# Kernel optimization log

Hardware: AMD Instinct MI355X
Metric: run time of the kernel (lower is better)

## Reference

```python
import jax, jax.numpy as jnp
import numpy as np

CHANNELS = 256

def setup_inputs() -> dict:
    key = jax.random.key(0)
    k1, k2, k3, k4 = jax.random.split(key, 4)
    B, C, N = 16, CHANNELS, 2048
    x = jax.random.normal(k1, (B, C, N), dtype=jnp.float32)
    # Conv1d(C, C, 1) weights are [C_out, C_in] after squeezing kernel dim.
    scale = 1.0 / np.sqrt(C)
    Wqk = jax.random.uniform(k2, (C, C), dtype=jnp.float32, minval=-scale, maxval=scale)  # shared q/k weight
    Wv = jax.random.uniform(k3, (C, C), dtype=jnp.float32, minval=-scale, maxval=scale)
    bv = jax.random.uniform(k4, (C,), dtype=jnp.float32, minval=-scale, maxval=scale)
    return {"x": x, "Wqk": Wqk, "Wv": Wv, "bv": bv}

def reference(x, Wqk, Wv, bv):
    # x: [B, C, N]; q_conv and k_conv share Wqk (tied in the torch module)
    C = x.shape[1]
    dk = jnp.asarray(C, x.dtype) ** 0.5
    x_q = jnp.einsum('oc,bcn->bno', Wqk, x)          # [B, N, C]
    x_k = jnp.einsum('oc,bcn->bon', Wqk, x)          # [B, C, N]
    x_v = jnp.einsum('oc,bcn->bon', Wv, x) + bv[None, :, None]  # [B, C, N]
    energy = jnp.einsum('bnc,bcm->bnm', x_q, x_k)    # [B, N, N]
    attention = jax.nn.softmax(energy, axis=-1)
    # offset-attention renorm: divide by column sums (dim=1), then by sqrt(C)
    attention = attention / (1e-9 + attention.sum(axis=1, keepdims=True))
    attention = attention / dk
    out = jnp.einsum('bcn,bnm->bcm', x_v, attention)  # [B, C, N]
    return out
```

## Files before the change

### kernel.cpp

```cpp
#include <hip/hip_runtime.h>


#define BB 16
#define CC 256
#define NN 2048

typedef float f4 __attribute__((ext_vector_type(4)));
typedef _Float16 h8 __attribute__((ext_vector_type(8)));
typedef _Float16 h4 __attribute__((ext_vector_type(4)));
typedef unsigned int u32;

#define SQRT_LOG2E 1.2011224087864498f
#define WSHIFT 128.0f
#define MFMA16(a, b, c) __builtin_amdgcn_mfma_f32_16x16x32_f16(a, b, c, 0, 0, 0)

__device__ __forceinline__ void glds16(const void* g, void* l) {
    __builtin_amdgcn_global_load_lds(
        (const __attribute__((address_space(1))) u32*)g,
        (__attribute__((address_space(3))) u32*)l, 16, 0, 0);
}

__global__ __launch_bounds__(64)
void convw_kernel(const float* __restrict__ Wqk, const float* __restrict__ Wv,
                  _Float16* __restrict__ Wh, _Float16* __restrict__ Wl)
{
    const int o = blockIdx.x;
    const int t = threadIdx.x;
    const float s = (o < CC) ? SQRT_LOG2E : 1.0f;
    const float* src = (o < CC) ? (Wqk + (size_t)o * CC) : (Wv + (size_t)(o - CC) * CC);
    f4 w = *(const f4*)(src + t * 4);
    h4 hh, hl;
#pragma unroll
    for (int q = 0; q < 4; ++q) {
        float v = s * w[q];
        _Float16 h = (_Float16)v;
        hh[q] = h;
        hl[q] = (_Float16)(v - (float)h);
    }
    *(h4*)(Wh + (size_t)o * CC + t * 4) = hh;
    *(h4*)(Wl + (size_t)o * CC + t * 4) = hl;
}

__global__ __launch_bounds__(256)
void transx_kernel(const float* __restrict__ X, _Float16* __restrict__ Xh,
                   _Float16* __restrict__ Xl)
{
    __shared__ float T[64][65];
    const int t = threadIdx.x;
    const int n0 = blockIdx.x * 64, c0 = blockIdx.y * 64, b = blockIdx.z;
    const float* Xb = X + (size_t)b * CC * NN;
    const int nq = (t & 15) * 4;
    const int cl = t >> 4;
#pragma unroll
    for (int cp = 0; cp < 64; cp += 16) {
        f4 v = *(const f4*)(Xb + (size_t)(c0 + cp + cl) * NN + n0 + nq);
#pragma unroll
        for (int q = 0; q < 4; ++q) T[nq + q][cp + cl] = v[q];
    }
    __syncthreads();
    const int n = t & 63, cq = (t >> 6) * 16;
    _Float16* dh = Xh + ((size_t)b * NN + n0 + n) * CC + c0 + cq;
    _Float16* dl = Xl + ((size_t)b * NN + n0 + n) * CC + c0 + cq;
#pragma unroll
    for (int g = 0; g < 2; ++g) {
        h8 hh, hl;
#pragma unroll
        for (int q = 0; q < 8; ++q) {
            float v = T[n][cq + g * 8 + q];
            _Float16 h = (_Float16)v;
            hh[q] = h;
            hl[q] = (_Float16)(v - (float)h);
        }
        *(h8*)(dh + g * 8) = hh;
        *(h8*)(dl + g * 8) = hl;
    }
}

__global__ __launch_bounds__(512, 4)
void proj_kernel(const _Float16* __restrict__ Xh, const _Float16* __restrict__ Xl,
                 const _Float16* __restrict__ Wh, const _Float16* __restrict__ Wl,
                 const float* __restrict__ bv, _Float16* __restrict__ Yt,
                 _Float16* __restrict__ V)
{
    __shared__ char L[65536];
    __shared__ float bbS[128];
    const int tid = threadIdx.x;
    const int lane = tid & 63, wid = tid >> 6;
    const int l15 = lane & 15, lg = lane >> 4;
    const int wo = wid >> 2, wn = wid & 3;
    const int n0 = blockIdx.x * 256;
    const int bo0 = blockIdx.y * 128;
    const int b = blockIdx.z;
    const bool isV = (blockIdx.y >= 2);
    const _Float16* xh = Xh + (size_t)b * NN * CC;
    const _Float16* xl = Xl + (size_t)b * NN * CC;

    if (isV && tid < 128) bbS[tid] = bv[bo0 - 256 + tid];

    f4 acc[4][4];
#pragma unroll
    for (int i = 0; i < 4; ++i)
#pragma unroll
        for (int j = 0; j < 4; ++j) acc[i][j] = (f4){0.f, 0.f, 0.f, 0.f};

    for (int c0 = 0; c0 < CC; c0 += 32) {
        __syncthreads();
#pragma unroll
        for (int q = 0; q < 2; ++q) {
            int id = tid * 2 + q;
            int arr = id >> 9, o = (id >> 2) & 127, s = id & 3;
            const _Float16* src = (arr ? Wl : Wh) + (size_t)(bo0 + o) * CC + c0 + s * 8;
            *(h8*)(L + arr * 10240 + o * 80 + s * 16) = *(const h8*)src;
        }
#pragma unroll
        for (int q = 0; q < 4; ++q) {
            int id = tid * 4 + q;
            int arr = id >> 10, n = (id >> 2) & 255, s = id & 3;
            const _Float16* src = (arr ? xl : xh) + (size_t)(n0 + n) * CC + c0 + s * 8;
            *(h8*)(L + 20480 + arr * 20480 + n * 80 + s * 16) = *(const h8*)src;
        }
        __syncthreads();
        h8 awh[4], awl[4];
#pragma unroll
        for (int oi = 0; oi < 4; ++oi) {
            int o = wo * 64 + oi * 16 + l15;
            awh[oi] = *(const h8*)(L + o * 80 + lg * 16);
            awl[oi] = *(const h8*)(L + 10240 + o * 80 + lg * 16);
        }
#pragma unroll
        for (int nj = 0; nj < 4; ++nj) {
            int n = wn * 64 + nj * 16 + l15;
            h8 bxh = *(const h8*)(L + 20480 + n * 80 + lg * 16);
            h8 bxl = *(const h8*)(L + 40960 + n * 80 + lg * 16);
#pragma unroll
            for (int oi = 0; oi < 4; ++oi) {
                acc[oi][nj] = MFMA16(awh[oi], bxh, acc[oi][nj]);
                acc[oi][nj] = MFMA16(awh[oi], bxl, acc[oi][nj]);
                acc[oi][nj] = MFMA16(awl[oi], bxh, acc[oi][nj]);
            }
        }
    }
    __syncthreads();
    if (!isV) {
#pragma unroll
        for (int oi = 0; oi < 4; ++oi)
#pragma unroll
            for (int nj = 0; nj < 4; ++nj) {
                int n = wn * 64 + nj * 16 + l15;
                int o = wo * 64 + oi * 16 + lg * 4;
                h4 r;
#pragma unroll
                for (int q = 0; q < 4; ++q) r[q] = (_Float16)acc[oi][nj][q];
                *(h4*)(L + n * 256 + ((o * 2) ^ ((n & 7) << 4))) = r;
            }
        __syncthreads();
        int n = tid >> 1, oh = (tid & 1) * 64;
        _Float16* dst = Yt + ((size_t)b * NN + n0 + n) * CC + bo0 + oh;
#pragma unroll
        for (int k = 0; k < 8; ++k)
            *(h8*)(dst + k * 8) = *(const h8*)(L + n * 256 + (((oh + k * 8) * 2) ^ ((n & 7) << 4)));
    } else {
#pragma unroll
        for (int oi = 0; oi < 4; ++oi)
#pragma unroll
            for (int nj = 0; nj < 4; ++nj) {
                int n = wn * 64 + nj * 16 + l15;
                int ob = wo * 64 + oi * 16 + lg * 4;
                f4 bb4 = *(const f4*)&bbS[ob];
#pragma unroll
                for (int r = 0; r < 4; ++r) {
                    int o = ob + r;
                    *(_Float16*)(L + o * 512 + ((n * 2) ^ ((o & 7) << 4))) =
                        (_Float16)(acc[oi][nj][r] + bb4[r]);
                }
            }
        __syncthreads();
        int o = tid >> 2, nq = (tid & 3) * 64;
        _Float16* dst = V + ((size_t)b * CC + bo0 - 256 + o) * NN + n0 + nq;
#pragma unroll
        for (int k = 0; k < 8; ++k)
            *(h8*)(dst + k * 8) = *(const h8*)(L + o * 512 + (((nq + k * 8) * 2) ^ ((o & 7) << 4)));
    }
}

__global__ __launch_bounds__(512, 4)
void rowsum_kernel(const _Float16* __restrict__ Yt, float* __restrict__ Rsum)
{
    __shared__ char As[16384];
    __shared__ char Bs[16384];
    __shared__ float rowred[128][2];
    __shared__ float colred[128][4];
    const int tid = threadIdx.x, lane = tid & 63, wid = tid >> 6;
    const int l15 = lane & 15, lg = lane >> 4;
    const int wn = wid >> 1, wm = wid & 1;
    int idx = blockIdx.x, I = 0;
    while (idx >= 16 - I) { idx -= 16 - I; ++I; }
    const int J = I + idx;
    const int b = blockIdx.y;
    const int nI0 = I * 128, nJ0 = J * 128;
    const char* Yb = (const char*)(Yt + (size_t)b * NN * CC);

    f4 eacc[2][4];
#pragma unroll
    for (int i = 0; i < 2; ++i)
#pragma unroll
        for (int j = 0; j < 4; ++j) eacc[i][j] = (f4){0.f, 0.f, 0.f, 0.f};

    for (int c0 = 0; c0 < CC; c0 += 64) {
        __syncthreads();
#pragma unroll
        for (int q = 0; q < 2; ++q) {
            int sid = q * 512 + tid;
            int n = sid >> 3, s = sid & 7;
            glds16(Yb + (size_t)(nI0 + n) * 512 + c0 * 2 + ((s * 16) ^ ((n & 7) << 4)),
                   As + sid * 16);
        }
#pragma unroll
        for (int q = 0; q < 2; ++q) {
            int sid = q * 512 + tid;
            int m = sid >> 3, s = sid & 7;
            glds16(Yb + (size_t)(nJ0 + m) * 512 + c0 * 2 + ((s * 16) ^ ((m & 7) << 4)),
                   Bs + sid * 16);
        }
        __syncthreads();
#pragma unroll
        for (int kk = 0; kk < 2; ++kk) {
            h8 a[2], bmf[4];
#pragma unroll
            for (int nt = 0; nt < 2; ++nt) {
                int n = wn * 32 + nt * 16 + l15;
                a[nt] = *(const h8*)(As + n * 128 + ((kk * 64 + lg * 16) ^ ((n & 7) << 4)));
            }
#pragma unroll
            for (int mt = 0; mt < 4; ++mt) {
                int m = wm * 64 + mt * 16 + l15;
                bmf[mt] = *(const h8*)(Bs + m * 128 + ((kk * 64 + lg * 16) ^ ((m & 7) << 4)));
            }
#pragma unroll
            for (int nt = 0; nt < 2; ++nt)
#pragma unroll
                for (int mt = 0; mt < 4; ++mt)
                    eacc[nt][mt] = MFMA16(a[nt], bmf[mt], eacc[nt][mt]);
        }
    }
    float rowp[2][4];
    float colp[4] = {0.f, 0.f, 0.f, 0.f};
#pragma unroll
    for (int nt = 0; nt < 2; ++nt)
#pragma unroll
        for (int r = 0; r < 4; ++r) rowp[nt][r] = 0.f;
#pragma unroll
    for (int nt = 0; nt < 2; ++nt)
#pragma unroll
        for (int mt = 0; mt < 4; ++mt)
#pragma unroll
            for (int r = 0; r < 4; ++r) {
                float p = __builtin_amdgcn_exp2f(eacc[nt][mt][r] - WSHIFT);
                rowp[nt][r] += p;
                colp[mt] += p;
            }
#pragma unroll
    for (int nt = 0; nt < 2; ++nt)
#pragma unroll
        for (int r = 0; r < 4; ++r) {
            float v = rowp[nt][r];
            v += __shfl_xor(v, 1); v += __shfl_xor(v, 2);
            v += __shfl_xor(v, 4); v += __shfl_xor(v, 8);
            if (l15 == 0) rowred[wn * 32 + nt * 16 + lg * 4 + r][wm] = v;
        }
#pragma unroll
    for (int mt = 0; mt < 4; ++mt) {
        float v = colp[mt];
        v += __shfl_xor(v, 16); v += __shfl_xor(v, 32);
        if (lg == 0) colred[wm * 64 + mt * 16 + l15][wn] = v;
    }
    __syncthreads();
    if (tid < 128)
        atomicAdd(&Rsum[(size_t)b * NN + nI0 + tid], rowred[tid][0] + rowred[tid][1]);
    if (I != J && tid >= 128 && tid < 256) {
        int m = tid - 128;
        atomicAdd(&Rsum[(size_t)b * NN + nJ0 + m],
                  colred[m][0] + colred[m][1] + colred[m][2] + colred[m][3]);
    }
}

__global__ __launch_bounds__(512, 2)
void out2_kernel(const _Float16* __restrict__ Yt, const _Float16* __restrict__ V,
                 const float* __restrict__ Rsum, float* __restrict__ Out)
{
    __shared__ char stage[49152];
    __shared__ char wT[65536];
    __shared__ float rinvS[256];
    __shared__ float colred[128][4];
    __shared__ float colS[128];

    const int tid = threadIdx.x, lane = tid & 63, wid = tid >> 6;
    const int l15 = lane & 15, lg = lane >> 4;
    const int wn = wid >> 1, wm = wid & 1;
    const int id = blockIdx.x;
    const int xcd = id & 7, j = id >> 3;
    const int b = xcd * 2 + (j >> 4);
    const int gm0 = (j & 15) * 128;
    const char* Yb = (const char*)(Yt + (size_t)b * NN * CC);
    const char* Vb = (const char*)(V + (size_t)b * CC * NN);

    f4 oacc[4][4];
#pragma unroll
    for (int i = 0; i < 4; ++i)
#pragma unroll
        for (int jj = 0; jj < 4; ++jj) oacc[i][jj] = (f4){0.f, 0.f, 0.f, 0.f};
    float colp[4] = {0.f, 0.f, 0.f, 0.f};

    for (int gn0 = 0; gn0 < NN; gn0 += 256) {
        f4 eacc[4][4];
#pragma unroll
        for (int i = 0; i < 4; ++i)
#pragma unroll
            for (int jj = 0; jj < 4; ++jj) eacc[i][jj] = (f4){0.f, 0.f, 0.f, 0.f};

        for (int c0 = 0; c0 < CC; c0 += 64) {
            __syncthreads();
            if (c0 == 0 && tid < 256)
                rinvS[tid] = 1.0f / Rsum[(size_t)b * NN + gn0 + tid];
#pragma unroll
            for (int q = 0; q < 4; ++q) {
                int sid = q * 512 + tid;
                int n = sid >> 3, s = sid & 7;
                glds16(Yb + (size_t)(gn0 + n) * 512 + c0 * 2 + ((s * 16) ^ ((n & 7) << 4)),
                       stage + sid * 16);
            }
#pragma unroll
            for (int q = 0; q < 2; ++q) {
                int sid = q * 512 + tid;
                int m = sid >> 3, s = sid & 7;
                glds16(Yb + (size_t)(gm0 + m) * 512 + c0 * 2 + ((s * 16) ^ ((m & 7) << 4)),
                       stage + 32768 + sid * 16);
            }
            __syncthreads();
#pragma unroll
            for (int kk = 0; kk < 2; ++kk) {
                h8 a[4], bmf[4];
#pragma unroll
                for (int nt = 0; nt < 4; ++nt) {
                    int n = wn * 64 + nt * 16 + l15;
                    a[nt] = *(const h8*)(stage + n * 128 + ((kk * 64 + lg * 16) ^ ((n & 7) << 4)));
                }
#pragma unroll
                for (int mt = 0; mt < 4; ++mt) {
                    int m = wm * 64 + mt * 16 + l15;
                    bmf[mt] = *(const h8*)(stage + 32768 + m * 128 + ((kk * 64 + lg * 16) ^ ((m & 7) << 4)));
                }
#pragma unroll
                for (int nt = 0; nt < 4; ++nt)
#pragma unroll
                    for (int mt = 0; mt < 4; ++mt)
                        eacc[nt][mt] = MFMA16(a[nt], bmf[mt], eacc[nt][mt]);
            }
        }

#pragma unroll
        for (int nt = 0; nt < 4; ++nt)
#pragma unroll
            for (int mt = 0; mt < 4; ++mt) {
                const int nl = wn * 64 + nt * 16 + lg * 4;
                const int m = wm * 64 + mt * 16 + l15;
                f4 e = eacc[nt][mt];
                f4 rv = *(const f4*)&rinvS[nl];
                float w0 = __builtin_amdgcn_exp2f(e[0] - WSHIFT) * rv[0];
                float w1 = __builtin_amdgcn_exp2f(e[1] - WSHIFT) * rv[1];
                float w2 = __builtin_amdgcn_exp2f(e[2] - WSHIFT) * rv[2];
                float w3 = __builtin_amdgcn_exp2f(e[3] - WSHIFT) * rv[3];
                colp[mt] += w0 + w1 + w2 + w3;
                h4 hw;
                hw[0] = (_Float16)w0; hw[1] = (_Float16)w1;
                hw[2] = (_Float16)w2; hw[3] = (_Float16)w3;
                *(h4*)(wT + m * 512 + ((nl * 2) ^ ((m & 7) << 4))) = hw;
            }
        __syncthreads();

        for (int kc = 0; kc < 4; ++kc) {
            if (kc) __syncthreads();
#pragma unroll
            for (int q = 0; q < 4; ++q) {
                int sid = q * 512 + tid;
                int c = sid >> 3, s = sid & 7;
                glds16(Vb + (size_t)c * (NN * 2) + (gn0 + kc * 64) * 2 + ((s * 16) ^ ((c & 7) << 4)),
                       stage + sid * 16);
            }
            __syncthreads();
#pragma unroll
            for (int kk = 0; kk < 2; ++kk) {
                h8 aw[4], bvf[4];
#pragma unroll
                for (int mt = 0; mt < 4; ++mt) {
                    int m = wm * 64 + mt * 16 + l15;
                    aw[mt] = *(const h8*)(wT + m * 512 + ((kc * 128 + kk * 64 + lg * 16) ^ ((m & 7) << 4)));
                }
#pragma unroll
                for (int ct = 0; ct < 4; ++ct) {
                    int c = wn * 64 + ct * 16 + l15;
                    bvf[ct] = *(const h8*)(stage + c * 128 + ((kk * 64 + lg * 16) ^ ((c & 7) << 4)));
                }
#pragma unroll
                for (int mt = 0; mt < 4; ++mt)
#pragma unroll
                    for (int ct = 0; ct < 4; ++ct)
                        oacc[mt][ct] = MFMA16(aw[mt], bvf[ct], oacc[mt][ct]);
            }
        }
    }

#pragma unroll
    for (int mt = 0; mt < 4; ++mt) {
        float v = colp[mt];
        v += __shfl_xor(v, 16); v += __shfl_xor(v, 32);
        if (lg == 0) colred[wm * 64 + mt * 16 + l15][wn] = v;
    }
    __syncthreads();
    if (tid < 128) {
        float s = colred[tid][0] + colred[tid][1] + colred[tid][2] + colred[tid][3];
        colS[tid] = 1.0f / ((1e-9f + s) * 16.0f);
    }
    __syncthreads();
#pragma unroll
    for (int mt = 0; mt < 4; ++mt) {
        const int m0 = wm * 64 + mt * 16 + lg * 4;
        f4 sc = *(const f4*)&colS[m0];
#pragma unroll
        for (int ct = 0; ct < 4; ++ct) {
            const int c = wn * 64 + ct * 16 + l15;
            f4 r;
#pragma unroll
            for (int q = 0; q < 4; ++q) r[q] = oacc[mt][ct][q] * sc[q];
            *(f4*)(Out + ((size_t)b * CC + c) * NN + gm0 + m0) = r;
        }
    }
}

extern "C" void kernel_launch(void* const* d_in, const int* in_sizes, int n_in,
                              void* d_out, int out_size, void* d_ws, size_t ws_size,
                              hipStream_t stream)
{
    const float* x   = (const float*)d_in[0];
    const float* Wqk = (const float*)d_in[1];
    const float* Wv  = (const float*)d_in[2];
    const float* bv  = (const float*)d_in[3];
    float* out = (float*)d_out;

    const size_t NE = (size_t)BB * NN * CC;
    _Float16* xh = (_Float16*)d_ws;
    _Float16* xl = xh + NE;
    _Float16* wh = xl + NE;
    _Float16* wl = wh + (size_t)512 * CC;
    _Float16* yt = wl + (size_t)512 * CC;
    _Float16* v  = yt + NE;
    float* rsum  = (float*)(v + NE);

    hipMemsetAsync(rsum, 0, (size_t)BB * NN * sizeof(float), stream);

    convw_kernel<<<dim3(512), dim3(64), 0, stream>>>(Wqk, Wv, wh, wl);
    transx_kernel<<<dim3(NN / 64, CC / 64, BB), dim3(256), 0, stream>>>(x, xh, xl);
    proj_kernel<<<dim3(NN / 256, 4, BB), dim3(512), 0, stream>>>(xh, xl, wh, wl, bv, yt, v);
    rowsum_kernel<<<dim3(136, BB), dim3(512), 0, stream>>>(yt, rsum);
    out2_kernel<<<dim3(256), dim3(512), 0, stream>>>(yt, v, rsum, out);
}
```

Baseline: 269.6 us.

## Halve output tiles in proj and attention kernels, use async LDS loads in proj

The proj kernel now uses 128-wide N tiles with 64-deep K steps and loads its operands through global_load_lds with an XOR-swizzled layout, replacing register-staged copies. The out2 kernel's query-column tile shrinks from 128 to 64, which doubles the grid to 512 blocks, cuts LDS use, and allows 4 blocks per CU. The aim is more parallelism and occupancy across the CUs in place of a grid of only 256 blocks. In exchange, the key-side energy recompute and the V tile loads are spread over half as many output columns per block, so redundant work and memory traffic per output rise.

```diff
diff --git a/kernel.cpp b/kernel.cpp
--- a/kernel.cpp
+++ b/kernel.cpp
@@ -88,56 +88,77 @@
     const int lane = tid & 63, wid = tid >> 6;
     const int l15 = lane & 15, lg = lane >> 4;
     const int wo = wid >> 2, wn = wid & 3;
-    const int n0 = blockIdx.x * 256;
+    const int n0 = blockIdx.x * 128;
     const int bo0 = blockIdx.y * 128;
     const int b = blockIdx.z;
     const bool isV = (blockIdx.y >= 2);
-    const _Float16* xh = Xh + (size_t)b * NN * CC;
-    const _Float16* xl = Xl + (size_t)b * NN * CC;
+    const char* xhB = (const char*)(Xh + (size_t)b * NN * CC);
+    const char* xlB = (const char*)(Xl + (size_t)b * NN * CC);
+    const char* whB = (const char*)Wh;
+    const char* wlB = (const char*)Wl;
 
     if (isV && tid < 128) bbS[tid] = bv[bo0 - 256 + tid];
 
-    f4 acc[4][4];
+    f4 acc[4][2];
 #pragma unroll
     for (int i = 0; i < 4; ++i)
 #pragma unroll
-        for (int j = 0; j < 4; ++j) acc[i][j] = (f4){0.f, 0.f, 0.f, 0.f};
-
-    for (int c0 = 0; c0 < CC; c0 += 32) {
-        __syncthreads();
-#pragma unroll
-        for (int q = 0; q < 2; ++q) {
-            int id = tid * 2 + q;
-            int arr = id >> 9, o = (id >> 2) & 127, s = id & 3;
-            const _Float16* src = (arr ? Wl : Wh) + (size_t)(bo0 + o) * CC + c0 + s * 8;
-            *(h8*)(L + arr * 10240 + o * 80 + s * 16) = *(const h8*)src;
-        }
-#pragma unroll
-        for (int q = 0; q < 4; ++q) {
-            int id = tid * 4 + q;
-            int arr = id >> 10, n = (id >> 2) & 255, s = id & 3;
-            const _Float16* src = (arr ? xl : xh) + (size_t)(n0 + n) * CC + c0 + s * 8;
-            *(h8*)(L + 20480 + arr * 20480 + n * 80 + s * 16) = *(const h8*)src;
-        }
-        __syncthreads();
-        h8 awh[4], awl[4];
-#pragma unroll
-        for (int oi = 0; oi < 4; ++oi) {
-            int o = wo * 64 + oi * 16 + l15;
-            awh[oi] = *(const h8*)(L + o * 80 + lg * 16);
-            awl[oi] = *(const h8*)(L + 10240 + o * 80 + lg * 16);
-        }
-#pragma unroll
-        for (int nj = 0; nj < 4; ++nj) {
-            int n = wn * 64 + nj * 16 + l15;
-            h8 bxh = *(const h8*)(L + 20480 + n * 80 + lg * 16);
-            h8 bxl = *(const h8*)(L + 40960 + n * 80 + lg * 16);
+        for (int j = 0; j < 2; ++j) acc[i][j] = (f4){0.f, 0.f, 0.f, 0.f};
+
+    for (int c0 = 0; c0 < CC; c0 += 64) {
+        __syncthreads();
+#pragma unroll
+        for (int q = 0; q < 2; ++q) {
+            int sid = q * 512 + tid;
+            int o = sid >> 3, s = sid & 7;
+            glds16(whB + (size_t)(bo0 + o) * 512 + c0 * 2 + ((s * 16) ^ ((o & 7) << 4)),
+                   L + sid * 16);
+        }
+#pragma unroll
+        for (int q = 0; q < 2; ++q) {
+            int sid = q * 512 + tid;
+            int o = sid >> 3, s = sid & 7;
+            glds16(wlB + (size_t)(bo0 + o) * 512 + c0 * 2 + ((s * 16) ^ ((o & 7) << 4)),
+                   L + 16384 + sid * 16);
+        }
+#pragma unroll
+        for (int q = 0; q < 2; ++q) {
+            int sid = q * 512 + tid;
+            int n = sid >> 3, s = sid & 7;
+            glds16(xhB + (size_t)(n0 + n) * 512 + c0 * 2 + ((s * 16) ^ ((n & 7) << 4)),
+                   L + 32768 + sid * 16);
+        }
+#pragma unroll
+        for (int q = 0; q < 2; ++q) {
+            int sid = q * 512 + tid;
+            int n = sid >> 3, s = sid & 7;
+            glds16(xlB + (size_t)(n0 + n) * 512 + c0 * 2 + ((s * 16) ^ ((n & 7) << 4)),
+                   L + 49152 + sid * 16);
+        }
+        __syncthreads();
+#pragma unroll
+        for (int kk = 0; kk < 2; ++kk) {
+            h8 awh[4], awl[4], bxh[2], bxl[2];
 #pragma unroll
             for (int oi = 0; oi < 4; ++oi) {
-                acc[oi][nj] = MFMA16(awh[oi], bxh, acc[oi][nj]);
-                acc[oi][nj] = MFMA16(awh[oi], bxl, acc[oi][nj]);
-                acc[oi][nj] = MFMA16(awl[oi], bxh, acc[oi][nj]);
-            }
+                int o = wo * 64 + oi * 16 + l15;
+                awh[oi] = *(const h8*)(L + o * 128 + ((kk * 64 + lg * 16) ^ ((o & 7) << 4)));
+                awl[oi] = *(const h8*)(L + 16384 + o * 128 + ((kk * 64 + lg * 16) ^ ((o & 7) << 4)));
+            }
+#pragma unroll
+            for (int nj = 0; nj < 2; ++nj) {
+                int n = wn * 32 + nj * 16 + l15;
+                bxh[nj] = *(const h8*)(L + 32768 + n * 128 + ((kk * 64 + lg * 16) ^ ((n & 7) << 4)));
+                bxl[nj] = *(const h8*)(L + 49152 + n * 128 + ((kk * 64 + lg * 16) ^ ((n & 7) << 4)));
+            }
+#pragma unroll
+            for (int oi = 0; oi < 4; ++oi)
+#pragma unroll
+                for (int nj = 0; nj < 2; ++nj) {
+                    acc[oi][nj] = MFMA16(awh[oi], bxh[nj], acc[oi][nj]);
+                    acc[oi][nj] = MFMA16(awh[oi], bxl[nj], acc[oi][nj]);
+                    acc[oi][nj] = MFMA16(awl[oi], bxh[nj], acc[oi][nj]);
+                }
         }
     }
     __syncthreads();
@@ -145,8 +166,8 @@
 #pragma unroll
         for (int oi = 0; oi < 4; ++oi)
 #pragma unroll
-            for (int nj = 0; nj < 4; ++nj) {
-                int n = wn * 64 + nj * 16 + l15;
+            for (int nj = 0; nj < 2; ++nj) {
+                int n = wn * 32 + nj * 16 + l15;
                 int o = wo * 64 + oi * 16 + lg * 4;
                 h4 r;
 #pragma unroll
@@ -154,32 +175,32 @@
                 *(h4*)(L + n * 256 + ((o * 2) ^ ((n & 7) << 4))) = r;
             }
         __syncthreads();
-        int n = tid >> 1, oh = (tid & 1) * 64;
-        _Float16* dst = Yt + ((size_t)b * NN + n0 + n) * CC + bo0 + oh;
-#pragma unroll
-        for (int k = 0; k < 8; ++k)
-            *(h8*)(dst + k * 8) = *(const h8*)(L + n * 256 + (((oh + k * 8) * 2) ^ ((n & 7) << 4)));
+        int n = tid >> 2, oq = (tid & 3) * 32;
+        _Float16* dst = Yt + ((size_t)b * NN + n0 + n) * CC + bo0 + oq;
+#pragma unroll
+        for (int k = 0; k < 4; ++k)
+            *(h8*)(dst + k * 8) = *(const h8*)(L + n * 256 + (((oq + k * 8) * 2) ^ ((n & 7) << 4)));
     } else {
 #pragma unroll
         for (int oi = 0; oi < 4; ++oi)
 #pragma unroll
-            for (int nj = 0; nj < 4; ++nj) {
-                int n = wn * 64 + nj * 16 + l15;
+            for (int nj = 0; nj < 2; ++nj) {
+                int n = wn * 32 + nj * 16 + l15;
                 int ob = wo * 64 + oi * 16 + lg * 4;
                 f4 bb4 = *(const f4*)&bbS[ob];
 #pragma unroll
                 for (int r = 0; r < 4; ++r) {
                     int o = ob + r;
-                    *(_Float16*)(L + o * 512 + ((n * 2) ^ ((o & 7) << 4))) =
+                    *(_Float16*)(L + o * 256 + ((n * 2) ^ ((o & 7) << 4))) =
                         (_Float16)(acc[oi][nj][r] + bb4[r]);
                 }
             }
         __syncthreads();
-        int o = tid >> 2, nq = (tid & 3) * 64;
+        int o = tid >> 2, nq = (tid & 3) * 32;
         _Float16* dst = V + ((size_t)b * CC + bo0 - 256 + o) * NN + n0 + nq;
 #pragma unroll
-        for (int k = 0; k < 8; ++k)
-            *(h8*)(dst + k * 8) = *(const h8*)(L + o * 512 + (((nq + k * 8) * 2) ^ ((o & 7) << 4)));
+        for (int k = 0; k < 4; ++k)
+            *(h8*)(dst + k * 8) = *(const h8*)(L + o * 256 + (((nq + k * 8) * 2) ^ ((o & 7) << 4)));
     }
 }
 
@@ -284,39 +305,39 @@
     }
 }
 
-__global__ __launch_bounds__(512, 2)
+__global__ __launch_bounds__(512, 4)
 void out2_kernel(const _Float16* __restrict__ Yt, const _Float16* __restrict__ V,
                  const float* __restrict__ Rsum, float* __restrict__ Out)
 {
-    __shared__ char stage[49152];
-    __shared__ char wT[65536];
+    __shared__ char stage[40960];
+    __shared__ char wT[32768];
     __shared__ float rinvS[256];
-    __shared__ float colred[128][4];
-    __shared__ float colS[128];
+    __shared__ float colred[64][4];
+    __shared__ float colS[64];
 
     const int tid = threadIdx.x, lane = tid & 63, wid = tid >> 6;
     const int l15 = lane & 15, lg = lane >> 4;
     const int wn = wid >> 1, wm = wid & 1;
     const int id = blockIdx.x;
     const int xcd = id & 7, j = id >> 3;
-    const int b = xcd * 2 + (j >> 4);
-    const int gm0 = (j & 15) * 128;
+    const int b = xcd * 2 + (j >> 5);
+    const int gm0 = (j & 31) * 64;
     const char* Yb = (const char*)(Yt + (size_t)b * NN * CC);
     const char* Vb = (const char*)(V + (size_t)b * CC * NN);
 
-    f4 oacc[4][4];
-#pragma unroll
-    for (int i = 0; i < 4; ++i)
+    f4 oacc[2][4];
+#pragma unroll
+    for (int i = 0; i < 2; ++i)
 #pragma unroll
         for (int jj = 0; jj < 4; ++jj) oacc[i][jj] = (f4){0.f, 0.f, 0.f, 0.f};
-    float colp[4] = {0.f, 0.f, 0.f, 0.f};
+    float colp[2] = {0.f, 0.f};
 
     for (int gn0 = 0; gn0 < NN; gn0 += 256) {
-        f4 eacc[4][4];
+        f4 eacc[4][2];
 #pragma unroll
         for (int i = 0; i < 4; ++i)
 #pragma unroll
-            for (int jj = 0; jj < 4; ++jj) eacc[i][jj] = (f4){0.f, 0.f, 0.f, 0.f};
+            for (int jj = 0; jj < 2; ++jj) eacc[i][jj] = (f4){0.f, 0.f, 0.f, 0.f};
 
         for (int c0 = 0; c0 < CC; c0 += 64) {
             __syncthreads();
@@ -329,31 +350,29 @@
                 glds16(Yb + (size_t)(gn0 + n) * 512 + c0 * 2 + ((s * 16) ^ ((n & 7) << 4)),
                        stage + sid * 16);
             }
-#pragma unroll
-            for (int q = 0; q < 2; ++q) {
-                int sid = q * 512 + tid;
-                int m = sid >> 3, s = sid & 7;
+            {
+                int m = tid >> 3, s = tid & 7;
                 glds16(Yb + (size_t)(gm0 + m) * 512 + c0 * 2 + ((s * 16) ^ ((m & 7) << 4)),
-                       stage + 32768 + sid * 16);
+                       stage + 32768 + tid * 16);
             }
             __syncthreads();
 #pragma unroll
             for (int kk = 0; kk < 2; ++kk) {
-                h8 a[4], bmf[4];
+                h8 a[4], bmf[2];
 #pragma unroll
                 for (int nt = 0; nt < 4; ++nt) {
                     int n = wn * 64 + nt * 16 + l15;
                     a[nt] = *(const h8*)(stage + n * 128 + ((kk * 64 + lg * 16) ^ ((n & 7) << 4)));
                 }
 #pragma unroll
-                for (int mt = 0; mt < 4; ++mt) {
-                    int m = wm * 64 + mt * 16 + l15;
+                for (int mt = 0; mt < 2; ++mt) {
+                    int m = wm * 32 + mt * 16 + l15;
                     bmf[mt] = *(const h8*)(stage + 32768 + m * 128 + ((kk * 64 + lg * 16) ^ ((m & 7) << 4)));
                 }
 #pragma unroll
                 for (int nt = 0; nt < 4; ++nt)
 #pragma unroll
-                    for (int mt = 0; mt < 4; ++mt)
+                    for (int mt = 0; mt < 2; ++mt)
                         eacc[nt][mt] = MFMA16(a[nt], bmf[mt], eacc[nt][mt]);
             }
         }
@@ -361,9 +380,9 @@
 #pragma unroll
         for (int nt = 0; nt < 4; ++nt)
 #pragma unroll
-            for (int mt = 0; mt < 4; ++mt) {
+            for (int mt = 0; mt < 2; ++mt) {
                 const int nl = wn * 64 + nt * 16 + lg * 4;
-                const int m = wm * 64 + mt * 16 + l15;
+                const int m = wm * 32 + mt * 16 + l15;
                 f4 e = eacc[nt][mt];
                 f4 rv = *(const f4*)&rinvS[nl];
                 float w0 = __builtin_amdgcn_exp2f(e[0] - WSHIFT) * rv[0];
@@ -390,10 +409,10 @@
             __syncthreads();
 #pragma unroll
             for (int kk = 0; kk < 2; ++kk) {
-                h8 aw[4], bvf[4];
-#pragma unroll
-                for (int mt = 0; mt < 4; ++mt) {
-                    int m = wm * 64 + mt * 16 + l15;
+                h8 aw[2], bvf[4];
+#pragma unroll
+                for (int mt = 0; mt < 2; ++mt) {
+                    int m = wm * 32 + mt * 16 + l15;
                     aw[mt] = *(const h8*)(wT + m * 512 + ((kc * 128 + kk * 64 + lg * 16) ^ ((m & 7) << 4)));
                 }
 #pragma unroll
@@ -402,7 +421,7 @@
                     bvf[ct] = *(const h8*)(stage + c * 128 + ((kk * 64 + lg * 16) ^ ((c & 7) << 4)));
                 }
 #pragma unroll
-                for (int mt = 0; mt < 4; ++mt)
+                for (int mt = 0; mt < 2; ++mt)
 #pragma unroll
                     for (int ct = 0; ct < 4; ++ct)
                         oacc[mt][ct] = MFMA16(aw[mt], bvf[ct], oacc[mt][ct]);
@@ -411,20 +430,20 @@
     }
 
 #pragma unroll
-    for (int mt = 0; mt < 4; ++mt) {
+    for (int mt = 0; mt < 2; ++mt) {
         float v = colp[mt];
         v += __shfl_xor(v, 16); v += __shfl_xor(v, 32);
-        if (lg == 0) colred[wm * 64 + mt * 16 + l15][wn] = v;
+        if (lg == 0) colred[wm * 32 + mt * 16 + l15][wn] = v;
     }
     __syncthreads();
-    if (tid < 128) {
+    if (tid < 64) {
         float s = colred[tid][0] + colred[tid][1] + colred[tid][2] + colred[tid][3];
         colS[tid] = 1.0f / ((1e-9f + s) * 16.0f);
     }
     __syncthreads();
 #pragma unroll
-    for (int mt = 0; mt < 4; ++mt) {
-        const int m0 = wm * 64 + mt * 16 + lg * 4;
+    for (int mt = 0; mt < 2; ++mt) {
+        const int m0 = wm * 32 + mt * 16 + lg * 4;
         f4 sc = *(const f4*)&colS[m0];
 #pragma unroll
         for (int ct = 0; ct < 4; ++ct) {
@@ -460,7 +479,7 @@
 
     convw_kernel<<<dim3(512), dim3(64), 0, stream>>>(Wqk, Wv, wh, wl);
     transx_kernel<<<dim3(NN / 64, CC / 64, BB), dim3(256), 0, stream>>>(x, xh, xl);
-    proj_kernel<<<dim3(NN / 256, 4, BB), dim3(512), 0, stream>>>(xh, xl, wh, wl, bv, yt, v);
+    proj_kernel<<<dim3(NN / 128, 4, BB), dim3(512), 0, stream>>>(xh, xl, wh, wl, bv, yt, v);
     rowsum_kernel<<<dim3(136, BB), dim3(512), 0, stream>>>(yt, rsum);
-    out2_kernel<<<dim3(256), dim3(512), 0, stream>>>(yt, v, rsum, out);
-}
+    out2_kernel<<<dim3(512), dim3(512), 0, stream>>>(yt, v, rsum, out);
+}
```

After: 268.5 us. About the same (-0.4%).
